# Performance work log

Measured on AMD Instinct MI355X. Metric: run time of the kernel, lower is better.

Reference implementation:

```python
import jax, jax.numpy as jnp
import numpy as np

N_ENTITY = 100000
H_DIM = 512
N_ROWS = 262144
ALPHA = 0.5          # EMA rate for fast state
GATE_TH = 0.5        # gate_threshold buffer
GATE_SCALE = 5.0     # gate_scale buffer
LN_EPS = 1e-5


def setup_inputs() -> dict:
    key = jax.random.key(0)
    k1, k2, k3, k4, k5 = jax.random.split(key, 5)
    entity_emb = jax.random.normal(k1, (N_ROWS, H_DIM), dtype=jnp.float32)
    entity_ids = jax.random.randint(k2, (N_ROWS,), 0, N_ENTITY, dtype=jnp.int64)
    slow_state = 0.1 * jax.random.normal(k3, (N_ENTITY, H_DIM), dtype=jnp.float32)
    fast_state = 0.1 * jax.random.normal(k4, (N_ENTITY, H_DIM), dtype=jnp.float32)
    # torch nn.Linear(2h, h): weight shape (h, 2h), y = x @ W.T + b
    W = jax.random.normal(k5, (H_DIM, 2 * H_DIM), dtype=jnp.float32) * 0.02
    b = jnp.zeros((H_DIM,), dtype=jnp.float32)
    return {"entity_emb": entity_emb, "slow_state": slow_state,
            "fast_state": fast_state, "W": W, "b": b, "entity_ids": entity_ids}


def _layer_norm(x):
    mu = jnp.mean(x, axis=-1, keepdims=True)
    var = jnp.mean(jnp.square(x - mu), axis=-1, keepdims=True)
    return (x - mu) * jax.lax.rsqrt(var + LN_EPS)


def reference(entity_emb, slow_state, fast_state, W, b, entity_ids):
    # ---- fuse_with_state (gate path) ----
    state = slow_state[entity_ids]                                   # (N, h) gather
    is_active = (jnp.sum(jnp.abs(state), axis=-1, keepdims=True) > 1e-6).astype(entity_emb.dtype)
    h_state = _layer_norm(state)
    gate_in = jnp.concatenate([entity_emb, h_state], axis=-1)        # (N, 2h)
    z = jax.nn.sigmoid(gate_in @ W.T + b)                            # (N, h)
    fused = z * entity_emb + (1.0 - z) * h_state
    out = is_active * fused + (1.0 - is_active) * entity_emb

    # ---- writeback (no-grad in torch; scatter-reduce EMA + norm-gated slow update) ----
    ctx = jax.lax.stop_gradient(out)
    ids = entity_ids
    counts = jax.ops.segment_sum(jnp.ones((ctx.shape[0],), ctx.dtype), ids,
                                 num_segments=N_ENTITY)              # (E,)
    ctx_sum = jax.ops.segment_sum(ctx, ids, num_segments=N_ENTITY)   # (E, h)
    ctx_mean = ctx_sum / jnp.clip(counts, 1.0)[:, None]
    touched = (counts > 0)[:, None]
    new_fast_all = (1.0 - ALPHA) * fast_state + ALPHA * ctx_mean
    new_fast = jnp.where(touched, new_fast_all, fast_state)
    diff = new_fast - slow_state
    delta = jnp.linalg.norm(diff, axis=-1, keepdims=True)
    gate = jax.nn.sigmoid(GATE_SCALE * (delta - GATE_TH))
    new_slow = jnp.where(touched, slow_state + gate * diff, slow_state)
    return out, new_fast, new_slow
```

## Files before the change

kernel.cpp:

```cpp
#include <hip/hip_runtime.h>
#include <hip/hip_bf16.h>
#include <cstdint>

#define NROWS 262144
#define HDIM  512
#define NENT  100000
#define SCAN_NBLK ((NENT + 1023) / 1024)

typedef __attribute__((ext_vector_type(4))) float  f32x4;
typedef __attribute__((ext_vector_type(8))) short  bf16x8;

static __device__ __forceinline__ unsigned short f2bf(float x) {
    unsigned u = __float_as_uint(x);
    u += 0x7FFF + ((u >> 16) & 1);
    return (unsigned short)(u >> 16);
}

__global__ void pack_w_kernel(const float* __restrict__ W, unsigned short* __restrict__ Wp) {
    int g    = blockIdx.x * 256 + threadIdx.x;
    int lane = g & 63;
    int task = g >> 6;
    int nt   = task >> 5;
    int kt   = task & 31;
    int col  = nt * 16 + (lane & 15);
    int k    = kt * 32 + ((lane >> 4) << 3);
    const float* src = W + (size_t)col * 1024 + k;
    f32x4 v0 = *(const f32x4*)(src);
    f32x4 v1 = *(const f32x4*)(src + 4);
    bf16x8 ov;
#pragma unroll
    for (int i = 0; i < 4; ++i) {
        ov[i]     = (short)f2bf(v0[i]);
        ov[4 + i] = (short)f2bf(v1[i]);
    }
    *(bf16x8*)(Wp + (size_t)g * 8) = ov;
}

__global__ __launch_bounds__(256) void count_kernel(const int* __restrict__ ids,
                                                    unsigned* __restrict__ counts) {
    int r = blockIdx.x * 256 + threadIdx.x;
    if (r < NROWS) atomicAdd(&counts[ids[r]], 1u);
}

__global__ __launch_bounds__(1024) void scan1_kernel(const unsigned* __restrict__ counts,
                                                     unsigned* __restrict__ off,
                                                     unsigned* __restrict__ bsums) {
    __shared__ unsigned tmp[1024];
    int i = blockIdx.x * 1024 + threadIdx.x;
    unsigned v = (i < NENT) ? counts[i] : 0u;
    tmp[threadIdx.x] = v;
    __syncthreads();
#pragma unroll
    for (int o = 1; o < 1024; o <<= 1) {
        unsigned a = (threadIdx.x >= o) ? tmp[threadIdx.x - o] : 0u;
        __syncthreads();
        tmp[threadIdx.x] += a;
        __syncthreads();
    }
    if (i < NENT) off[i] = tmp[threadIdx.x] - v;
    if (threadIdx.x == 1023) bsums[blockIdx.x] = tmp[1023];
}

__global__ void scan2_kernel(unsigned* __restrict__ bsums) {
    if (threadIdx.x == 0 && blockIdx.x == 0) {
        unsigned s = 0;
        for (int i = 0; i < SCAN_NBLK; ++i) { unsigned t = bsums[i]; bsums[i] = s; s += t; }
    }
}

__global__ __launch_bounds__(1024) void scan3_kernel(unsigned* __restrict__ off,
                                                     const unsigned* __restrict__ bsums,
                                                     unsigned* __restrict__ cursor) {
    int i = blockIdx.x * 1024 + threadIdx.x;
    if (i < NENT) {
        unsigned o = off[i] + bsums[blockIdx.x];
        off[i] = o;
        cursor[i] = o;
    }
    if (i == 0) off[NENT] = NROWS;
}

__global__ __launch_bounds__(256) void fill_kernel(const int* __restrict__ ids,
                                                   unsigned* __restrict__ cursor,
                                                   int* __restrict__ rowidx) {
    int r = blockIdx.x * 256 + threadIdx.x;
    if (r < NROWS) {
        unsigned p = atomicAdd(&cursor[ids[r]], 1u);
        rowidx[p] = r;
    }
}

__global__ __launch_bounds__(512) void fuse_kernel(
    const float* __restrict__ emb, const float* __restrict__ slow,
    const unsigned short* __restrict__ Wp, const float* __restrict__ bias,
    const int* __restrict__ ids, float* __restrict__ out)
{
    __shared__ unsigned short aLds[8 * 512];
    __shared__ float muS[64], rsS[64], actS[64], bS[512];
    __shared__ int idS[64];

    const int t    = threadIdx.x;
    const int w    = t >> 6;
    const int lane = t & 63;
    const int brow = blockIdx.x * 64;

    if (t < 128) ((f32x4*)bS)[t] = ((const f32x4*)bias)[t];

    for (int rr = 0; rr < 8; ++rr) {
        int row = w * 8 + rr;
        int id  = ids[brow + row];
        const float* sp = slow + (size_t)id * HDIM;
        f32x4 v0 = ((const f32x4*)sp)[lane * 2];
        f32x4 v1 = ((const f32x4*)sp)[lane * 2 + 1];
        float s = 0.f, s2 = 0.f, sa = 0.f;
#pragma unroll
        for (int i = 0; i < 4; ++i) {
            s  += v0[i] + v1[i];
            s2 += v0[i] * v0[i] + v1[i] * v1[i];
            sa += fabsf(v0[i]) + fabsf(v1[i]);
        }
#pragma unroll
        for (int m = 32; m >= 1; m >>= 1) {
            s  += __shfl_xor(s, m);
            s2 += __shfl_xor(s2, m);
            sa += __shfl_xor(sa, m);
        }
        if (lane == 0) {
            float mu  = s * (1.f / HDIM);
            float var = s2 * (1.f / HDIM) - mu * mu;
            muS[row]  = mu;
            rsS[row]  = rsqrtf(var + 1e-5f);
            actS[row] = (sa > 1e-6f) ? 1.f : 0.f;
            idS[row]  = id;
        }
    }
    __syncthreads();

    const int rowS = t >> 3;
    const int kc   = t & 7;
    const float* embRow = emb + (size_t)(brow + rowS) * HDIM;
    const float* stRow  = slow + (size_t)idS[rowS] * HDIM;
    const float muR = muS[rowS], rsR = rsS[rowS];

    const int rt_s = rowS >> 4, rl_s = rowS & 15;
    const int kt_s = kc >> 2,  kg_s = kc & 3;
    unsigned short* aDst = &aLds[(kt_s * 4 + rt_s) * 512 + (kg_s * 16 + (rl_s ^ (kg_s << 1))) * 8];
    const int kgr = lane >> 4, rlr = lane & 15;
    const int posr = kgr * 16 + (rlr ^ (kgr << 1));

    const int c0 = w * 64;
    f32x4 zero4 = {0.f, 0.f, 0.f, 0.f};
    f32x4 acc[4][4];
#pragma unroll
    for (int i = 0; i < 4; ++i)
#pragma unroll
        for (int j = 0; j < 4; ++j) acc[i][j] = zero4;

    for (int ks = 0; ks < 16; ++ks) {
        f32x4 x0, x1;
        int kb = ks * 64 + kc * 8;
        if (ks < 8) {
            x0 = *(const f32x4*)(embRow + kb);
            x1 = *(const f32x4*)(embRow + kb + 4);
        } else {
            x0 = *(const f32x4*)(stRow + kb - 512);
            x1 = *(const f32x4*)(stRow + kb - 512 + 4);
#pragma unroll
            for (int i = 0; i < 4; ++i) {
                x0[i] = (x0[i] - muR) * rsR;
                x1[i] = (x1[i] - muR) * rsR;
            }
        }
        __syncthreads();
        bf16x8 av;
#pragma unroll
        for (int i = 0; i < 4; ++i) {
            av[i]     = (short)f2bf(x0[i]);
            av[4 + i] = (short)f2bf(x1[i]);
        }
        *(bf16x8*)aDst = av;
        __syncthreads();

#pragma unroll
        for (int kk = 0; kk < 2; ++kk) {
            bf16x8 a0 = *(const bf16x8*)&aLds[(kk * 4 + 0) * 512 + posr * 8];
            bf16x8 a1 = *(const bf16x8*)&aLds[(kk * 4 + 1) * 512 + posr * 8];
            bf16x8 a2 = *(const bf16x8*)&aLds[(kk * 4 + 2) * 512 + posr * 8];
            bf16x8 a3 = *(const bf16x8*)&aLds[(kk * 4 + 3) * 512 + posr * 8];
            int kt32 = ks * 2 + kk;
#pragma unroll
            for (int ct = 0; ct < 4; ++ct) {
                int ntile = (c0 >> 4) + ct;
                bf16x8 bfr = *(const bf16x8*)(Wp + ((size_t)(ntile * 32 + kt32) * 64 + lane) * 8);
                acc[0][ct] = __builtin_amdgcn_mfma_f32_16x16x32_bf16(bfr, a0, acc[0][ct], 0, 0, 0);
                acc[1][ct] = __builtin_amdgcn_mfma_f32_16x16x32_bf16(bfr, a1, acc[1][ct], 0, 0, 0);
                acc[2][ct] = __builtin_amdgcn_mfma_f32_16x16x32_bf16(bfr, a2, acc[2][ct], 0, 0, 0);
                acc[3][ct] = __builtin_amdgcn_mfma_f32_16x16x32_bf16(bfr, a3, acc[3][ct], 0, 0, 0);
            }
        }
    }

#pragma unroll
    for (int rt = 0; rt < 4; ++rt) {
        int rowl = rt * 16 + (lane & 15);
        int grow = brow + rowl;
        int id   = idS[rowl];
        float mu = muS[rowl], rs = rsS[rowl], act = actS[rowl];
        const float* embP  = emb  + (size_t)grow * HDIM;
        const float* slowP = slow + (size_t)id * HDIM;
        float*       outP  = out  + (size_t)grow * HDIM;
#pragma unroll
        for (int ct = 0; ct < 4; ++ct) {
            int col0 = c0 + ct * 16 + ((lane >> 4) << 2);
            f32x4 bv = *(const f32x4*)&bS[col0];
            f32x4 ev = *(const f32x4*)(embP + col0);
            f32x4 sv = *(const f32x4*)(slowP + col0);
            f32x4 o;
#pragma unroll
            for (int r = 0; r < 4; ++r) {
                float logit = acc[rt][ct][r] + bv[r];
                float z  = 1.f / (1.f + __expf(-logit));
                float h  = (sv[r] - mu) * rs;
                float fused = z * ev[r] + (1.f - z) * h;
                o[r] = (act > 0.f) ? fused : ev[r];
            }
            *(f32x4*)(outP + col0) = o;
        }
    }
}

__global__ __launch_bounds__(256) void finalize_kernel(
    const float* __restrict__ fast, const float* __restrict__ slow,
    const float* __restrict__ out, const unsigned* __restrict__ off,
    const int* __restrict__ rowidx, float* __restrict__ nf, float* __restrict__ ns)
{
    int e = blockIdx.x * 4 + (threadIdx.x >> 6);
    if (e >= NENT) return;
    int lane = threadIdx.x & 63;
    size_t base = (size_t)e * HDIM + lane * 8;

    f32x4 f0 = *(const f32x4*)(fast + base), f1 = *(const f32x4*)(fast + base + 4);
    f32x4 l0 = *(const f32x4*)(slow + base), l1 = *(const f32x4*)(slow + base + 4);

    unsigned o0 = off[e], o1 = off[e + 1];
    int c = (int)(o1 - o0);

    if (c == 0) {
        *(f32x4*)(nf + base)     = f0;
        *(f32x4*)(nf + base + 4) = f1;
        *(f32x4*)(ns + base)     = l0;
        *(f32x4*)(ns + base + 4) = l1;
        return;
    }

    f32x4 s0 = {0.f, 0.f, 0.f, 0.f}, s1 = {0.f, 0.f, 0.f, 0.f};
    for (int j = 0; j < c; ++j) {
        int r = rowidx[o0 + j];
        const float* p = out + (size_t)r * HDIM + lane * 8;
        s0 += *(const f32x4*)p;
        s1 += *(const f32x4*)(p + 4);
    }

    float inv = 0.5f / (float)c;
    f32x4 n0, n1, d0, d1;
    float ss = 0.f;
#pragma unroll
    for (int i = 0; i < 4; ++i) {
        n0[i] = 0.5f * f0[i] + s0[i] * inv;
        n1[i] = 0.5f * f1[i] + s1[i] * inv;
        d0[i] = n0[i] - l0[i]; ss += d0[i] * d0[i];
        d1[i] = n1[i] - l1[i]; ss += d1[i] * d1[i];
    }
#pragma unroll
    for (int m = 32; m >= 1; m >>= 1) ss += __shfl_xor(ss, m);
    float delta = sqrtf(ss);
    float gate  = 1.f / (1.f + expf(-5.f * (delta - 0.5f)));

    f32x4 o0v, o1v;
#pragma unroll
    for (int i = 0; i < 4; ++i) {
        o0v[i] = l0[i] + gate * d0[i];
        o1v[i] = l1[i] + gate * d1[i];
    }
    *(f32x4*)(nf + base)     = n0;
    *(f32x4*)(nf + base + 4) = n1;
    *(f32x4*)(ns + base)     = o0v;
    *(f32x4*)(ns + base + 4) = o1v;
}

extern "C" void kernel_launch(void* const* d_in, const int* in_sizes, int n_in,
                              void* d_out, int out_size, void* d_ws, size_t ws_size,
                              hipStream_t stream) {
    const float* emb  = (const float*)d_in[0];
    const float* slow = (const float*)d_in[1];
    const float* fast = (const float*)d_in[2];
    const float* W    = (const float*)d_in[3];
    const float* bias = (const float*)d_in[4];
    const int*   ids  = (const int*)d_in[5];

    float* out = (float*)d_out;
    float* nf  = out + (size_t)NROWS * HDIM;
    float* ns  = nf + (size_t)NENT * HDIM;

    unsigned short* Wp   = (unsigned short*)d_ws;
    unsigned* counts     = (unsigned*)((char*)d_ws + (1u << 20));
    unsigned* off        = (unsigned*)((char*)d_ws + (1u << 20) + 512 * 1024);
    unsigned* bsums      = (unsigned*)((char*)d_ws + (2u << 20));
    int*      rowidx     = (int*)((char*)d_ws + (2u << 20) + 4096);

    hipMemsetAsync(counts, 0, (size_t)NENT * sizeof(unsigned), stream);

    pack_w_kernel<<<256, 256, 0, stream>>>(W, Wp);
    count_kernel<<<NROWS / 256, 256, 0, stream>>>(ids, counts);
    scan1_kernel<<<SCAN_NBLK, 1024, 0, stream>>>(counts, off, bsums);
    scan2_kernel<<<1, 64, 0, stream>>>(bsums);
    scan3_kernel<<<SCAN_NBLK, 1024, 0, stream>>>(off, bsums, counts);
    fill_kernel<<<NROWS / 256, 256, 0, stream>>>(ids, counts, rowidx);
    fuse_kernel<<<NROWS / 64, 512, 0, stream>>>(emb, slow, Wp, bias, ids, out);
    finalize_kernel<<<(NENT + 3) / 4, 256, 0, stream>>>(fast, slow, out, off, rowidx, nf, ns);
}
```

Baseline: 985.3 us.

## Stage weight tiles in LDS with double-buffered 128-row GEMM blocks

The gate GEMM is restructured into 1024-thread blocks covering 128 rows. Each K-phase's bf16 weight tile and activation tile are staged cooperatively into double-buffered LDS. The next phase's global loads are issued while the MFMAs for the current phase run, and the weight pack layout is made k-tile-major to match. This replaces per-wave global reads of the weight fragments, cuts one barrier per step and doubles weight reuse per block. The cost is higher LDS use, which limits occupancy, and heavier register pressure under the larger block size.

```diff
diff --git a/kernel.cpp b/kernel.cpp
--- a/kernel.cpp
+++ b/kernel.cpp
@@ -9,6 +9,7 @@
 
 typedef __attribute__((ext_vector_type(4))) float  f32x4;
 typedef __attribute__((ext_vector_type(8))) short  bf16x8;
+typedef __attribute__((ext_vector_type(4))) short  bf16x4;
 
 static __device__ __forceinline__ unsigned short f2bf(float x) {
     unsigned u = __float_as_uint(x);
@@ -19,9 +20,8 @@
 __global__ void pack_w_kernel(const float* __restrict__ W, unsigned short* __restrict__ Wp) {
     int g    = blockIdx.x * 256 + threadIdx.x;
     int lane = g & 63;
-    int task = g >> 6;
-    int nt   = task >> 5;
-    int kt   = task & 31;
+    int nt   = (g >> 6) & 31;
+    int kt   = g >> 11;
     int col  = nt * 16 + (lane & 15);
     int k    = kt * 32 + ((lane >> 4) << 3);
     const float* src = W + (size_t)col * 1024 + k;
@@ -90,19 +90,22 @@
     }
 }
 
-__global__ __launch_bounds__(512) void fuse_kernel(
+__global__ __launch_bounds__(1024, 4) void fuse_kernel(
     const float* __restrict__ emb, const float* __restrict__ slow,
     const unsigned short* __restrict__ Wp, const float* __restrict__ bias,
     const int* __restrict__ ids, float* __restrict__ out)
 {
-    __shared__ unsigned short aLds[8 * 512];
-    __shared__ float muS[64], rsS[64], actS[64], bS[512];
-    __shared__ int idS[64];
+    __shared__ unsigned short wLds[2][2048 * 8];
+    __shared__ unsigned short xLds[2][512 * 8];
+    __shared__ float muS[128], rsS[128], actS[128], bS[512];
+    __shared__ int idS[128];
 
     const int t    = threadIdx.x;
     const int w    = t >> 6;
     const int lane = t & 63;
-    const int brow = blockIdx.x * 64;
+    const int wm   = w >> 3;
+    const int wn   = w & 7;
+    const int brow = blockIdx.x * 128;
 
     if (t < 128) ((f32x4*)bS)[t] = ((const f32x4*)bias)[t];
 
@@ -136,19 +139,13 @@
     }
     __syncthreads();
 
-    const int rowS = t >> 3;
-    const int kc   = t & 7;
-    const float* embRow = emb + (size_t)(brow + rowS) * HDIM;
-    const float* stRow  = slow + (size_t)idS[rowS] * HDIM;
-    const float muR = muS[rowS], rsR = rsS[rowS];
-
-    const int rt_s = rowS >> 4, rl_s = rowS & 15;
-    const int kt_s = kc >> 2,  kg_s = kc & 3;
-    unsigned short* aDst = &aLds[(kt_s * 4 + rt_s) * 512 + (kg_s * 16 + (rl_s ^ (kg_s << 1))) * 8];
-    const int kgr = lane >> 4, rlr = lane & 15;
-    const int posr = kgr * 16 + (rlr ^ (kgr << 1));
-
-    const int c0 = w * 64;
+    const int xrow = t >> 3;
+    const int kloc = (t & 7) * 4;
+    const float* srcState = slow + (size_t)idS[xrow] * HDIM + kloc;
+    const float* srcEmb   = emb + (size_t)(brow + xrow) * HDIM + kloc;
+    const float muR = muS[xrow], rsR = rsS[xrow];
+    const int xByte = (((xrow >> 4) * 64 + (((kloc >> 3) << 4) | (xrow & 15))) << 4) + ((kloc & 7) << 1);
+
     f32x4 zero4 = {0.f, 0.f, 0.f, 0.f};
     f32x4 acc[4][4];
 #pragma unroll
@@ -156,53 +153,63 @@
 #pragma unroll
         for (int j = 0; j < 4; ++j) acc[i][j] = zero4;
 
-    for (int ks = 0; ks < 16; ++ks) {
-        f32x4 x0, x1;
-        int kb = ks * 64 + kc * 8;
-        if (ks < 8) {
-            x0 = *(const f32x4*)(embRow + kb);
-            x1 = *(const f32x4*)(embRow + kb + 4);
-        } else {
-            x0 = *(const f32x4*)(stRow + kb - 512);
-            x1 = *(const f32x4*)(stRow + kb - 512 + 4);
-#pragma unroll
-            for (int i = 0; i < 4; ++i) {
-                x0[i] = (x0[i] - muR) * rsR;
-                x1[i] = (x1[i] - muR) * rsR;
-            }
-        }
+#define ISSUE(ph, wr0, wr1, xr)                                          \
+    {   int ktW = ((ph) < 16) ? (16 + (ph)) : ((ph) - 16);               \
+        const bf16x8* wp = (const bf16x8*)(Wp + (size_t)ktW * 16384);    \
+        wr0 = wp[t];                                                     \
+        wr1 = wp[t + 1024];                                              \
+        const float* xp = ((ph) < 16) ? (srcState + (ph) * 32)           \
+                                      : (srcEmb + ((ph) - 16) * 32);     \
+        xr = *(const f32x4*)xp;                                          \
+    }
+
+#define COMMIT(ph, buf, wr0, wr1, xr)                                    \
+    {   ((bf16x8*)wLds[buf])[t]        = wr0;                            \
+        ((bf16x8*)wLds[buf])[t + 1024] = wr1;                            \
+        f32x4 y = xr;                                                    \
+        if ((ph) < 16) {                                                 \
+            _Pragma("unroll")                                            \
+            for (int i = 0; i < 4; ++i) y[i] = (y[i] - muR) * rsR;       \
+        }                                                                \
+        bf16x4 xv;                                                       \
+        _Pragma("unroll")                                                \
+        for (int i = 0; i < 4; ++i) xv[i] = (short)f2bf(y[i]);           \
+        *(bf16x4*)((char*)xLds[buf] + xByte) = xv;                       \
+    }
+
+    {   bf16x8 wr0, wr1; f32x4 xr;
+        ISSUE(0, wr0, wr1, xr);
+        COMMIT(0, 0, wr0, wr1, xr);
+    }
+    __syncthreads();
+
+    for (int ph = 0; ph < 32; ++ph) {
+        const int cur = ph & 1;
+        bf16x8 wr0, wr1; f32x4 xr;
+        if (ph < 31) ISSUE(ph + 1, wr0, wr1, xr);
+
+        bf16x8 wf0 = ((const bf16x8*)wLds[cur])[(wn * 4 + 0) * 64 + lane];
+        bf16x8 wf1 = ((const bf16x8*)wLds[cur])[(wn * 4 + 1) * 64 + lane];
+        bf16x8 wf2 = ((const bf16x8*)wLds[cur])[(wn * 4 + 2) * 64 + lane];
+        bf16x8 wf3 = ((const bf16x8*)wLds[cur])[(wn * 4 + 3) * 64 + lane];
+#pragma unroll
+        for (int rt = 0; rt < 4; ++rt) {
+            bf16x8 xf = ((const bf16x8*)xLds[cur])[(wm * 4 + rt) * 64 + lane];
+            acc[rt][0] = __builtin_amdgcn_mfma_f32_16x16x32_bf16(wf0, xf, acc[rt][0], 0, 0, 0);
+            acc[rt][1] = __builtin_amdgcn_mfma_f32_16x16x32_bf16(wf1, xf, acc[rt][1], 0, 0, 0);
+            acc[rt][2] = __builtin_amdgcn_mfma_f32_16x16x32_bf16(wf2, xf, acc[rt][2], 0, 0, 0);
+            acc[rt][3] = __builtin_amdgcn_mfma_f32_16x16x32_bf16(wf3, xf, acc[rt][3], 0, 0, 0);
+        }
+
+        if (ph < 31) COMMIT(ph + 1, cur ^ 1, wr0, wr1, xr);
         __syncthreads();
-        bf16x8 av;
-#pragma unroll
-        for (int i = 0; i < 4; ++i) {
-            av[i]     = (short)f2bf(x0[i]);
-            av[4 + i] = (short)f2bf(x1[i]);
-        }
-        *(bf16x8*)aDst = av;
-        __syncthreads();
-
-#pragma unroll
-        for (int kk = 0; kk < 2; ++kk) {
-            bf16x8 a0 = *(const bf16x8*)&aLds[(kk * 4 + 0) * 512 + posr * 8];
-            bf16x8 a1 = *(const bf16x8*)&aLds[(kk * 4 + 1) * 512 + posr * 8];
-            bf16x8 a2 = *(const bf16x8*)&aLds[(kk * 4 + 2) * 512 + posr * 8];
-            bf16x8 a3 = *(const bf16x8*)&aLds[(kk * 4 + 3) * 512 + posr * 8];
-            int kt32 = ks * 2 + kk;
-#pragma unroll
-            for (int ct = 0; ct < 4; ++ct) {
-                int ntile = (c0 >> 4) + ct;
-                bf16x8 bfr = *(const bf16x8*)(Wp + ((size_t)(ntile * 32 + kt32) * 64 + lane) * 8);
-                acc[0][ct] = __builtin_amdgcn_mfma_f32_16x16x32_bf16(bfr, a0, acc[0][ct], 0, 0, 0);
-                acc[1][ct] = __builtin_amdgcn_mfma_f32_16x16x32_bf16(bfr, a1, acc[1][ct], 0, 0, 0);
-                acc[2][ct] = __builtin_amdgcn_mfma_f32_16x16x32_bf16(bfr, a2, acc[2][ct], 0, 0, 0);
-                acc[3][ct] = __builtin_amdgcn_mfma_f32_16x16x32_bf16(bfr, a3, acc[3][ct], 0, 0, 0);
-            }
-        }
-    }
+    }
+#undef ISSUE
+#undef COMMIT
 
 #pragma unroll
     for (int rt = 0; rt < 4; ++rt) {
-        int rowl = rt * 16 + (lane & 15);
+        int rowl = wm * 64 + rt * 16 + (lane & 15);
         int grow = brow + rowl;
         int id   = idS[rowl];
         float mu = muS[rowl], rs = rsS[rowl], act = actS[rowl];
@@ -211,7 +218,7 @@
         float*       outP  = out  + (size_t)grow * HDIM;
 #pragma unroll
         for (int ct = 0; ct < 4; ++ct) {
-            int col0 = c0 + ct * 16 + ((lane >> 4) << 2);
+            int col0 = wn * 64 + ct * 16 + ((lane >> 4) << 2);
             f32x4 bv = *(const f32x4*)&bS[col0];
             f32x4 ev = *(const f32x4*)(embP + col0);
             f32x4 sv = *(const f32x4*)(slowP + col0);
@@ -316,6 +323,6 @@
     scan2_kernel<<<1, 64, 0, stream>>>(bsums);
     scan3_kernel<<<SCAN_NBLK, 1024, 0, stream>>>(off, bsums, counts);
     fill_kernel<<<NROWS / 256, 256, 0, stream>>>(ids, counts, rowidx);
-    fuse_kernel<<<NROWS / 64, 512, 0, stream>>>(emb, slow, Wp, bias, ids, out);
+    fuse_kernel<<<NROWS / 128, 1024, 0, stream>>>(emb, slow, Wp, bias, ids, out);
     finalize_kernel<<<(NENT + 3) / 4, 256, 0, stream>>>(fast, slow, out, off, rowidx, nf, ns);
 }
```

Result: slower. 1.032 ms (+4.7%).
